# Kernel optimization log

Hardware: AMD Instinct MI355X
Metric: run time of the kernel (lower is better)

Reference implementation:

```python
import jax, jax.numpy as jnp
import numpy as np

NUM_EMBEDDINGS = 1024
EMBEDDING_DIM = 256
COMMITMENT_COST = 0.25
DECAY = 0.99
EPSILON = 1e-05


def setup_inputs() -> dict:
    key = jax.random.key(0)
    k1, k2, k3 = jax.random.split(key, 3)
    inputs = jax.random.normal(k1, (64, 1024, EMBEDDING_DIM), dtype=jnp.float32)
    embed_w = jax.random.uniform(
        k2, (NUM_EMBEDDINGS, EMBEDDING_DIM), dtype=jnp.float32,
        minval=-1.0 / NUM_EMBEDDINGS, maxval=1.0 / NUM_EMBEDDINGS)
    ema_cluster_size = jnp.ones((NUM_EMBEDDINGS,), dtype=jnp.float32)
    ema_w = jax.random.normal(k3, (NUM_EMBEDDINGS, EMBEDDING_DIM), dtype=jnp.float32)
    return {"inputs": inputs, "embed_w": embed_w,
            "ema_cluster_size": ema_cluster_size, "ema_w": ema_w}


def reference(inputs, embed_w, ema_cluster_size, ema_w):
    K, D = embed_w.shape
    flat = inputs.reshape(-1, D)  # [N, D]
    distances = (jnp.sum(flat * flat, axis=1, keepdims=True)
                 - 2.0 * flat @ embed_w.T
                 + jnp.sum(embed_w * embed_w, axis=1)[None, :])
    encoding_indices = jnp.argmin(distances, axis=1)  # [N]
    quantized = embed_w[encoding_indices].reshape(inputs.shape)

    # training-mode EMA updates (match torch buffer math; indices are constants)
    counts = jax.ops.segment_sum(
        jnp.ones_like(encoding_indices, dtype=inputs.dtype),
        encoding_indices, num_segments=K)  # == encodings.sum(0)
    dw = jax.ops.segment_sum(flat, encoding_indices, num_segments=K)  # == encodings.T @ flat
    new_cs = ema_cluster_size * DECAY + (1.0 - DECAY) * counts
    new_ema_w = ema_w * DECAY + (1.0 - DECAY) * dw
    n = jnp.sum(new_cs)
    new_cs = (new_cs + EPSILON) / (n + K * EPSILON) * n
    updated_embed = new_ema_w / new_cs[:, None]

    sg = jax.lax.stop_gradient
    e_latent_loss = jnp.mean((sg(quantized) - inputs) ** 2)
    q_latent_loss = jnp.mean((quantized - sg(inputs)) ** 2)
    loss = q_latent_loss + COMMITMENT_COST * e_latent_loss
    quantized_ste = inputs + sg(quantized - inputs)
    return (quantized_ste, loss, encoding_indices, new_cs, new_ema_w, updated_embed)
```

## Files before the change

### kernel.cpp

```cpp
#include <hip/hip_runtime.h>
#include <math.h>

#define NROWS 65536
#define D 256
#define K 1024
#define CAP 8
#define SCAP 16
#define EPS 1e-3f

#define OFF_Q     0
#define OFF_LOSS  16777216
#define OFF_IDX   16777217
#define OFF_CS    16842753
#define OFF_EMAW  16843777
#define OFF_UPD   17105921

#define WS_HIST     0
#define WS_GC       4096
#define WS_OFFS     8192
#define WS_CURS     12288
#define WS_IDX      16384
#define WS_CNT      278528
#define WS_WROWS    540672
#define WS_ROWIDS   802816
#define WS_SQX      1064960
#define WS_SQE      1327104
#define WS_DW       1331200
#define WS_PACK     1331200
#define WS_LOSSP    2379776
#define WS_EBT      2387968
#define WS_CAND     2912256

typedef __attribute__((ext_vector_type(8))) short short8;
typedef __attribute__((ext_vector_type(8))) unsigned short ushort8;
typedef __attribute__((ext_vector_type(4))) float f32x4;

__device__ __forceinline__ unsigned short f2b(float f) {
    unsigned u = __builtin_bit_cast(unsigned, f);
    return (unsigned short)((u + 0x7fffu + ((u >> 16) & 1u)) >> 16);
}

__device__ __forceinline__ float dot_chain(const float4* __restrict__ xr,
                                           const float4* __restrict__ er) {
#pragma clang fp contract(off)
    float acc = 0.f;
#pragma unroll
    for (int g = 0; g < 8; ++g) {
        float4 xa[8], ea[8];
#pragma unroll
        for (int m = 0; m < 8; ++m) { xa[m] = xr[g * 8 + m]; ea[m] = er[g * 8 + m]; }
#pragma unroll
        for (int m = 0; m < 8; ++m) {
            acc = __builtin_fmaf(xa[m].x, ea[m].x, acc);
            acc = __builtin_fmaf(xa[m].y, ea[m].y, acc);
            acc = __builtin_fmaf(xa[m].z, ea[m].z, acc);
            acc = __builtin_fmaf(xa[m].w, ea[m].w, acc);
        }
    }
    return acc;
}

__global__ __launch_bounds__(256) void k_cvt(const float* __restrict__ ew,
                                             unsigned short* __restrict__ ebt,
                                             float* __restrict__ sqe)
{
#pragma clang fp contract(off)
    int t = blockIdx.x * 256 + threadIdx.x;
    int code = t >> 3, kc = t & 7;
    const float4* src = (const float4*)&ew[(size_t)code * 256 + kc * 32];
    unsigned short* dst = &ebt[((size_t)kc * 1024 + code) * 32];
    float4 f[8];
#pragma unroll
    for (int j = 0; j < 8; ++j) f[j] = src[j];
#pragma unroll
    for (int j = 0; j < 8; ++j) {
        ushort4 o;
        o.x = f2b(f[j].x); o.y = f2b(f[j].y); o.z = f2b(f[j].z); o.w = f2b(f[j].w);
        *(ushort4*)&dst[j * 4] = o;
    }
    float p[16];
#pragma unroll
    for (int m = 0; m < 4; ++m) {
        p[4*m+0] = f[m].x * f[m].x + f[m+4].x * f[m+4].x;
        p[4*m+1] = f[m].y * f[m].y + f[m+4].y * f[m+4].y;
        p[4*m+2] = f[m].z * f[m].z + f[m+4].z * f[m+4].z;
        p[4*m+3] = f[m].w * f[m].w + f[m+4].w * f[m+4].w;
    }
    float V[16];
#pragma unroll
    for (int l2 = 0; l2 < 16; ++l2) {
        float q = p[l2] + __shfl_xor(p[l2], 1);
        V[l2] = q + __shfl_xor(q, 2);
    }
    float t8[8];
#pragma unroll
    for (int l2 = 0; l2 < 8; ++l2) t8[l2] = V[l2] + V[l2 + 8];
    float u4[4];
#pragma unroll
    for (int l2 = 0; l2 < 4; ++l2) u4[l2] = t8[l2] + t8[l2 + 4];
    float h = (u4[0] + u4[2]) + (u4[1] + u4[3]);
    float sq = h + __shfl_xor(h, 4);
    if (kc == 0) sqe[code] = sq;
}

__global__ __launch_bounds__(256) void k_screen(
    const float* __restrict__ x, const unsigned short* __restrict__ ebt,
    const float* __restrict__ sqe, float* __restrict__ sqx_out,
    int* __restrict__ cnt, int* __restrict__ cand,
    int* __restrict__ idx_out, float* __restrict__ idxf_out,
    int* __restrict__ hist, int* __restrict__ wrows, int* __restrict__ gc,
    unsigned long long* __restrict__ packed)
{
    __shared__ unsigned short xs[32][264];
    __shared__ float red[32][4];
    __shared__ int lcnt[32];
    __shared__ float gmin[32];
    __shared__ int scand_c[32][SCAP];
    __shared__ float scand_s[32][SCAP];

    const int tid = threadIdx.x;
    const int wn = tid >> 6;
    const int l = tid & 63;
    const int row0 = blockIdx.x * 32;

    if (tid < 32) { lcnt[tid] = 0; gmin[tid] = 3.4e38f; }

    {
        const int row = tid >> 3, kq8 = tid & 7;
        const float4* src = (const float4*)&x[(size_t)(row0 + row) * 256 + kq8 * 32];
        float4 f[8];
#pragma unroll
        for (int j = 0; j < 8; ++j) f[j] = src[j];
#pragma unroll
        for (int j = 0; j < 8; ++j) {
            ushort4 o;
            o.x = f2b(f[j].x); o.y = f2b(f[j].y); o.z = f2b(f[j].z); o.w = f2b(f[j].w);
            *(ushort4*)&xs[row][kq8 * 32 + j * 4] = o;
        }
        float p[16];
#pragma unroll
        for (int m = 0; m < 4; ++m) {
            p[4*m+0] = f[m].x * f[m].x + f[m+4].x * f[m+4].x;
            p[4*m+1] = f[m].y * f[m].y + f[m+4].y * f[m+4].y;
            p[4*m+2] = f[m].z * f[m].z + f[m+4].z * f[m+4].z;
            p[4*m+3] = f[m].w * f[m].w + f[m+4].w * f[m+4].w;
        }
        float V[16];
#pragma unroll
        for (int l2 = 0; l2 < 16; ++l2) {
            float q = p[l2] + __shfl_xor(p[l2], 1);
            V[l2] = q + __shfl_xor(q, 2);
        }
        float t8[8];
#pragma unroll
        for (int l2 = 0; l2 < 8; ++l2) t8[l2] = V[l2] + V[l2 + 8];
        float u4[4];
#pragma unroll
        for (int l2 = 0; l2 < 4; ++l2) u4[l2] = t8[l2] + t8[l2 + 4];
        float h = (u4[0] + u4[2]) + (u4[1] + u4[3]);
        float sq = h + __shfl_xor(h, 4);
        if (kq8 == 0) sqx_out[row0 + row] = sq;
    }
    __syncthreads();

#pragma unroll 1
    for (int ct = 0; ct < 4; ++ct) {
        f32x4 acc[2][4];
#pragma unroll
        for (int mt = 0; mt < 2; ++mt)
#pragma unroll
            for (int nt = 0; nt < 4; ++nt) acc[mt][nt] = (f32x4)0.f;

#pragma unroll 2
        for (int kc = 0; kc < 8; ++kc) {
            short8 a[2], b[4];
#pragma unroll
            for (int nt = 0; nt < 4; ++nt)
                b[nt] = *(const short8*)&ebt[
                    ((size_t)kc * 1024 + ct * 256 + wn * 64 + nt * 16 + (l & 15)) * 32
                    + (l >> 4) * 8];
#pragma unroll
            for (int mt = 0; mt < 2; ++mt)
                a[mt] = *(const short8*)&xs[mt * 16 + (l & 15)][kc * 32 + (l >> 4) * 8];
#pragma unroll
            for (int mt = 0; mt < 2; ++mt)
#pragma unroll
                for (int nt = 0; nt < 4; ++nt)
                    acc[mt][nt] = __builtin_amdgcn_mfma_f32_16x16x32_bf16(
                        a[mt], b[nt], acc[mt][nt], 0, 0, 0);
        }

        float sev[4];
#pragma unroll
        for (int nt = 0; nt < 4; ++nt)
            sev[nt] = sqe[ct * 256 + wn * 64 + nt * 16 + (l & 15)];

#pragma unroll
        for (int mt = 0; mt < 2; ++mt)
#pragma unroll
            for (int q = 0; q < 4; ++q) {
                const int rw = mt * 16 + (l >> 4) * 4 + q;
                float v = 3.4e38f;
#pragma unroll
                for (int nt = 0; nt < 4; ++nt)
                    v = fminf(v, sev[nt] - 2.0f * acc[mt][nt][q]);
#pragma unroll
                for (int m = 1; m < 16; m <<= 1) v = fminf(v, __shfl_xor(v, m));
                if ((l & 15) == 0) red[rw][wn] = v;
            }
        __syncthreads();
        if (tid < 32)
            gmin[tid] = fminf(gmin[tid],
                              fminf(fminf(red[tid][0], red[tid][1]),
                                    fminf(red[tid][2], red[tid][3])));
#pragma unroll
        for (int mt = 0; mt < 2; ++mt)
#pragma unroll
            for (int q = 0; q < 4; ++q) {
                const int rw = mt * 16 + (l >> 4) * 4 + q;
                const float rm = fminf(fminf(red[rw][0], red[rw][1]),
                                       fminf(red[rw][2], red[rw][3])) + EPS;
#pragma unroll
                for (int nt = 0; nt < 4; ++nt) {
                    float s = sev[nt] - 2.0f * acc[mt][nt][q];
                    if (s <= rm) {
                        int c = ct * 256 + wn * 64 + nt * 16 + (l & 15);
                        int slot = atomicAdd(&lcnt[rw], 1);
                        if (slot < SCAP) { scand_c[rw][slot] = c; scand_s[rw][slot] = s; }
                    }
                }
            }
        __syncthreads();
    }
    if (tid < 32) {
        const int row = row0 + tid;
        const int m = lcnt[tid];
        if (m > SCAP) {
            cnt[row] = CAP + 1;
            packed[row] = ~0ULL;
            int p0 = atomicAdd(&gc[0], 1);
            wrows[p0] = row;
        } else {
            const float thr = gmin[tid] + EPS;
            int n = 0;
            int keep[CAP];
            for (int j = 0; j < m; ++j) {
                if (scand_s[tid][j] <= thr) {
                    if (n < CAP) keep[n] = scand_c[tid][j];
                    ++n;
                }
            }
            cnt[row] = n;
            if (n == 1) {
                idx_out[row] = keep[0];
                idxf_out[row] = (float)keep[0];
                atomicAdd(&hist[keep[0]], 1);
            } else {
                packed[row] = ~0ULL;
                int p0 = atomicAdd(&gc[0], 1);
                wrows[p0] = row;
                const int mm = n < CAP ? n : CAP;
                for (int s = 0; s < mm; ++s)
                    cand[(size_t)row * CAP + s] = keep[s];
            }
        }
    }
}

__global__ __launch_bounds__(256) void k_rescore(
    const float* __restrict__ x, const float* __restrict__ ew,
    const float* __restrict__ sqx, const float* __restrict__ sqe,
    const int* __restrict__ cnt, const int* __restrict__ cand,
    const int* __restrict__ wrows, const int* __restrict__ gc,
    unsigned long long* __restrict__ packed)
{
#pragma clang fp contract(off)
    const int nw = gc[0];
    const int total = nw * CAP;
    for (int i = blockIdx.x * 256 + threadIdx.x; i < total; i += gridDim.x * 256) {
        const int row = wrows[i >> 3];
        const int slot = i & (CAP - 1);
        const int n = cnt[row];
        const float sxr = sqx[row];
        const float4* xr = (const float4*)&x[(size_t)row * 256];
        if (n >= 2 && n <= CAP) {
            if (slot >= n) continue;
            const int c = cand[(size_t)row * CAP + slot];
            float acc = dot_chain(xr, (const float4*)&ew[(size_t)c * 256]);
            float d = (sxr - 2.0f * acc) + sqe[c];
            unsigned long long key =
                ((unsigned long long)__builtin_bit_cast(unsigned, d) << 32) | (unsigned)c;
            atomicMin(&packed[row], key);
        } else {
            float bd = 3.4e38f; int bc = 0x7fffffff;
            for (int c = slot; c < K; c += CAP) {
                float acc = dot_chain(xr, (const float4*)&ew[(size_t)c * 256]);
                float d = (sxr - 2.0f * acc) + sqe[c];
                if (d < bd || (d == bd && c < bc)) { bd = d; bc = c; }
            }
            unsigned long long key =
                ((unsigned long long)__builtin_bit_cast(unsigned, bd) << 32) | (unsigned)bc;
            atomicMin(&packed[row], key);
        }
    }
}

__global__ __launch_bounds__(256) void k_resolve(
    const int* __restrict__ wrows, const int* __restrict__ gc,
    const unsigned long long* __restrict__ packed,
    int* __restrict__ idx_out, float* __restrict__ idxf_out, int* __restrict__ hist)
{
    const int nw = gc[0];
    for (int i = blockIdx.x * 256 + threadIdx.x; i < nw; i += gridDim.x * 256) {
        const int row = wrows[i];
        const int c = (int)(packed[row] & 0xffffffffu);
        idx_out[row] = c;
        idxf_out[row] = (float)c;
        atomicAdd(&hist[c], 1);
    }
}

__global__ __launch_bounds__(1024) void k_prefix(
    const int* __restrict__ hist, int* __restrict__ offs, int* __restrict__ curs)
{
    __shared__ int tmp[1024];
    const int tid = threadIdx.x;
    const int h = hist[tid];
    tmp[tid] = h;
    __syncthreads();
    for (int off = 1; off < 1024; off <<= 1) {
        int v = (tid >= off) ? tmp[tid - off] : 0;
        __syncthreads();
        tmp[tid] += v;
        __syncthreads();
    }
    int ex = tmp[tid] - h;
    offs[tid] = ex;
    curs[tid] = ex;
}

__global__ __launch_bounds__(256) void k_fill(
    const int* __restrict__ idx_in, int* __restrict__ curs, int* __restrict__ rowids)
{
    int r = blockIdx.x * 256 + threadIdx.x;
    int c = idx_in[r];
    int slot = atomicAdd(&curs[c], 1);
    rowids[slot] = r;
}

__global__ __launch_bounds__(256) void k_dw(
    const float* __restrict__ x, const float* __restrict__ ew,
    const int* __restrict__ hist, const int* __restrict__ offs,
    const int* __restrict__ rowids,
    float* __restrict__ q_out, float* __restrict__ dw, double* __restrict__ lossp)
{
    const int c = blockIdx.x;
    const int tid = threadIdx.x;
    const int n = hist[c];
    const int base = offs[c];
    const float ev = ew[(size_t)c * 256 + tid];
    float acc = 0.f;
    float lsum = 0.f;
    for (int i = 0; i < n; ++i) {
        int row = rowids[base + i];
        float xv = x[(size_t)row * 256 + tid];
        q_out[(size_t)row * 256 + tid] = ev;
        acc += xv;
        float df = ev - xv;
        lsum += df * df;
    }
    dw[(size_t)c * 256 + tid] = acc;
    const int lane = tid & 63, wid = tid >> 6;
    __shared__ float wsum[4];
#pragma unroll
    for (int m = 1; m < 64; m <<= 1) lsum += __shfl_xor(lsum, m);
    if (lane == 0) wsum[wid] = lsum;
    __syncthreads();
    if (tid == 0)
        lossp[c] = (double)wsum[0] + wsum[1] + wsum[2] + wsum[3];
}

__global__ __launch_bounds__(1024) void k_finalize(
    const float* __restrict__ ema_cs, const int* __restrict__ hist,
    const double* __restrict__ lossp, float* __restrict__ out)
{
    __shared__ double red[1024];
    const int tid = threadIdx.x;
    float raw = ema_cs[tid] * 0.99f + 0.01f * (float)hist[tid];
    red[tid] = (double)raw;
    __syncthreads();
    for (int s = 512; s > 0; s >>= 1) {
        if (tid < s) red[tid] += red[tid + s];
        __syncthreads();
    }
    double n = red[0];
    __syncthreads();
    float csn = (raw + 1e-5f) * (float)(n / (n + 1024.0 * 1e-5));
    out[OFF_CS + tid] = csn;
    red[tid] = lossp[tid];
    __syncthreads();
    for (int s = 512; s > 0; s >>= 1) {
        if (tid < s) red[tid] += red[tid + s];
        __syncthreads();
    }
    if (tid == 0) out[OFF_LOSS] = (float)(red[0] * 1.25 / 16777216.0);
}

__global__ __launch_bounds__(256) void k_ema(
    const float* __restrict__ ema_w, const float* __restrict__ dw,
    const float* __restrict__ cs_out, float* __restrict__ out)
{
    int id = blockIdx.x * 256 + threadIdx.x;
    int k = id >> 8;
    float nw = ema_w[id] * 0.99f + 0.01f * dw[id];
    out[OFF_EMAW + id] = nw;
    out[OFF_UPD + id] = nw / cs_out[k];
}

extern "C" void kernel_launch(void* const* d_in, const int* in_sizes, int n_in,
                              void* d_out, int out_size, void* d_ws, size_t ws_size,
                              hipStream_t stream)
{
    const float* x      = (const float*)d_in[0];
    const float* ew     = (const float*)d_in[1];
    const float* ema_cs = (const float*)d_in[2];
    const float* ema_w  = (const float*)d_in[3];
    float* out = (float*)d_out;
    char* ws = (char*)d_ws;

    int*    hist    = (int*)(ws + WS_HIST);
    int*    gc      = (int*)(ws + WS_GC);
    int*    offs    = (int*)(ws + WS_OFFS);
    int*    curs    = (int*)(ws + WS_CURS);
    int*    idxi    = (int*)(ws + WS_IDX);
    int*    cnt     = (int*)(ws + WS_CNT);
    int*    wrows   = (int*)(ws + WS_WROWS);
    int*    rowids  = (int*)(ws + WS_ROWIDS);
    float*  sqx     = (float*)(ws + WS_SQX);
    float*  sqe     = (float*)(ws + WS_SQE);
    float*  dw      = (float*)(ws + WS_DW);
    unsigned long long* packed = (unsigned long long*)(ws + WS_PACK);
    double* lossp   = (double*)(ws + WS_LOSSP);
    unsigned short* ebt = (unsigned short*)(ws + WS_EBT);
    int*    cand    = (int*)(ws + WS_CAND);

    hipMemsetAsync(ws, 0, 4112, stream);
    hipLaunchKernelGGL(k_cvt, dim3(32), dim3(256), 0, stream, ew, ebt, sqe);
    hipLaunchKernelGGL(k_screen, dim3(NROWS / 32), dim3(256), 0, stream,
                       x, ebt, sqe, sqx, cnt, cand, idxi, out + OFF_IDX,
                       hist, wrows, gc, packed);
    hipLaunchKernelGGL(k_rescore, dim3(512), dim3(256), 0, stream,
                       x, ew, sqx, sqe, cnt, cand, wrows, gc, packed);
    hipLaunchKernelGGL(k_resolve, dim3(64), dim3(256), 0, stream,
                       wrows, gc, packed, idxi, out + OFF_IDX, hist);
    hipLaunchKernelGGL(k_prefix, dim3(1), dim3(1024), 0, stream, hist, offs, curs);
    hipLaunchKernelGGL(k_fill, dim3(NROWS / 256), dim3(256), 0, stream,
                       idxi, curs, rowids);
    hipLaunchKernelGGL(k_dw, dim3(K), dim3(256), 0, stream,
                       x, ew, hist, offs, rowids, out + OFF_Q, dw, lossp);
    hipLaunchKernelGGL(k_finalize, dim3(1), dim3(1024), 0, stream,
                       ema_cs, hist, lossp, out);
    hipLaunchKernelGGL(k_ema, dim3(1024), dim3(256), 0, stream,
                       ema_w, dw, out + OFF_CS, out);
}
```

Before: 196.2 us.

## Split per-code dw gather into 64-row work units to balance load

The gather/segment-sum kernel previously ran one block per code, so a code with many assigned rows serialized its whole gather in a single block. Codes are now split into chunks of up to 64 rows, and the chunk list is built in the prefix kernel. Each chunk writes a partial dw row and a loss partial, and the EMA kernel sums the partials per code. This adds a second scan, extra workspace traffic and a fixed grid of 2048 blocks, which is only correct if the chunk count never exceeds 2048.

```diff
diff --git a/kernel.cpp b/kernel.cpp
--- a/kernel.cpp
+++ b/kernel.cpp
@@ -19,17 +19,19 @@
 #define WS_GC       4096
 #define WS_OFFS     8192
 #define WS_CURS     12288
-#define WS_IDX      16384
-#define WS_CNT      278528
-#define WS_WROWS    540672
-#define WS_ROWIDS   802816
-#define WS_SQX      1064960
-#define WS_SQE      1327104
-#define WS_DW       1331200
-#define WS_PACK     1331200
-#define WS_LOSSP    2379776
-#define WS_EBT      2387968
-#define WS_CAND     2912256
+#define WS_UOFFS    16384
+#define WS_UNITS    20736
+#define WS_IDX      29184
+#define WS_CNT      291328
+#define WS_WROWS    553472
+#define WS_ROWIDS   815616
+#define WS_SQX      1077760
+#define WS_SQE      1339904
+#define WS_LOSSP    1344000
+#define WS_EBT      1360384
+#define WS_CAND     1884672
+#define WS_UDW      3981824
+#define WS_PACK     3981824
 
 typedef __attribute__((ext_vector_type(8))) short short8;
 typedef __attribute__((ext_vector_type(8))) unsigned short ushort8;
@@ -321,7 +323,8 @@
 }
 
 __global__ __launch_bounds__(1024) void k_prefix(
-    const int* __restrict__ hist, int* __restrict__ offs, int* __restrict__ curs)
+    const int* __restrict__ hist, int* __restrict__ offs, int* __restrict__ curs,
+    int* __restrict__ uoffs, int* __restrict__ units, double* __restrict__ lossp)
 {
     __shared__ int tmp[1024];
     const int tid = threadIdx.x;
@@ -337,6 +340,23 @@
     int ex = tmp[tid] - h;
     offs[tid] = ex;
     curs[tid] = ex;
+    __syncthreads();
+    const int uc = (h + 63) >> 6;
+    tmp[tid] = uc;
+    __syncthreads();
+    for (int off = 1; off < 1024; off <<= 1) {
+        int v = (tid >= off) ? tmp[tid - off] : 0;
+        __syncthreads();
+        tmp[tid] += v;
+        __syncthreads();
+    }
+    const int uex = tmp[tid] - uc;
+    uoffs[tid] = uex;
+    if (tid == 1023) uoffs[1024] = tmp[1023];
+    lossp[tid] = 0.0;
+    lossp[tid + 1024] = 0.0;
+    for (int j = 0; j < uc; ++j)
+        units[uex + j] = (j << 10) | tid;
 }
 
 __global__ __launch_bounds__(256) void k_fill(
@@ -351,17 +371,25 @@
 __global__ __launch_bounds__(256) void k_dw(
     const float* __restrict__ x, const float* __restrict__ ew,
     const int* __restrict__ hist, const int* __restrict__ offs,
+    const int* __restrict__ uoffs, const int* __restrict__ units,
     const int* __restrict__ rowids,
-    float* __restrict__ q_out, float* __restrict__ dw, double* __restrict__ lossp)
-{
-    const int c = blockIdx.x;
+    float* __restrict__ q_out, float* __restrict__ udw, double* __restrict__ lossp)
+{
+    const int U = uoffs[1024];
+    const int b = blockIdx.x;
+    if (b >= U) return;
+    const int u = units[b];
+    const int c = u & 1023;
+    const int j = u >> 10;
     const int tid = threadIdx.x;
     const int n = hist[c];
-    const int base = offs[c];
+    const int start = j << 6;
+    const int len = min(64, n - start);
+    const int base = offs[c] + start;
     const float ev = ew[(size_t)c * 256 + tid];
     float acc = 0.f;
     float lsum = 0.f;
-    for (int i = 0; i < n; ++i) {
+    for (int i = 0; i < len; ++i) {
         int row = rowids[base + i];
         float xv = x[(size_t)row * 256 + tid];
         q_out[(size_t)row * 256 + tid] = ev;
@@ -369,7 +397,7 @@
         float df = ev - xv;
         lsum += df * df;
     }
-    dw[(size_t)c * 256 + tid] = acc;
+    udw[(size_t)b * 256 + tid] = acc;
     const int lane = tid & 63, wid = tid >> 6;
     __shared__ float wsum[4];
 #pragma unroll
@@ -377,7 +405,7 @@
     if (lane == 0) wsum[wid] = lsum;
     __syncthreads();
     if (tid == 0)
-        lossp[c] = (double)wsum[0] + wsum[1] + wsum[2] + wsum[3];
+        lossp[b] = (double)wsum[0] + wsum[1] + wsum[2] + wsum[3];
 }
 
 __global__ __launch_bounds__(1024) void k_finalize(
@@ -397,7 +425,7 @@
     __syncthreads();
     float csn = (raw + 1e-5f) * (float)(n / (n + 1024.0 * 1e-5));
     out[OFF_CS + tid] = csn;
-    red[tid] = lossp[tid];
+    red[tid] = lossp[tid] + lossp[tid + 1024];
     __syncthreads();
     for (int s = 512; s > 0; s >>= 1) {
         if (tid < s) red[tid] += red[tid + s];
@@ -407,14 +435,19 @@
 }
 
 __global__ __launch_bounds__(256) void k_ema(
-    const float* __restrict__ ema_w, const float* __restrict__ dw,
+    const float* __restrict__ ema_w, const float* __restrict__ udw,
+    const int* __restrict__ uoffs,
     const float* __restrict__ cs_out, float* __restrict__ out)
 {
     int id = blockIdx.x * 256 + threadIdx.x;
-    int k = id >> 8;
-    float nw = ema_w[id] * 0.99f + 0.01f * dw[id];
+    int c = id >> 8;
+    int d = id & 255;
+    const int u0 = uoffs[c], u1 = uoffs[c + 1];
+    float s = 0.f;
+    for (int u = u0; u < u1; ++u) s += udw[(size_t)u * 256 + d];
+    float nw = ema_w[id] * 0.99f + 0.01f * s;
     out[OFF_EMAW + id] = nw;
-    out[OFF_UPD + id] = nw / cs_out[k];
+    out[OFF_UPD + id] = nw / cs_out[c];
 }
 
 extern "C" void kernel_launch(void* const* d_in, const int* in_sizes, int n_in,
@@ -432,13 +465,15 @@
     int*    gc      = (int*)(ws + WS_GC);
     int*    offs    = (int*)(ws + WS_OFFS);
     int*    curs    = (int*)(ws + WS_CURS);
+    int*    uoffs   = (int*)(ws + WS_UOFFS);
+    int*    units   = (int*)(ws + WS_UNITS);
     int*    idxi    = (int*)(ws + WS_IDX);
     int*    cnt     = (int*)(ws + WS_CNT);
     int*    wrows   = (int*)(ws + WS_WROWS);
     int*    rowids  = (int*)(ws + WS_ROWIDS);
     float*  sqx     = (float*)(ws + WS_SQX);
     float*  sqe     = (float*)(ws + WS_SQE);
-    float*  dw      = (float*)(ws + WS_DW);
+    float*  udw     = (float*)(ws + WS_UDW);
     unsigned long long* packed = (unsigned long long*)(ws + WS_PACK);
     double* lossp   = (double*)(ws + WS_LOSSP);
     unsigned short* ebt = (unsigned short*)(ws + WS_EBT);
@@ -453,13 +488,15 @@
                        x, ew, sqx, sqe, cnt, cand, wrows, gc, packed);
     hipLaunchKernelGGL(k_resolve, dim3(64), dim3(256), 0, stream,
                        wrows, gc, packed, idxi, out + OFF_IDX, hist);
-    hipLaunchKernelGGL(k_prefix, dim3(1), dim3(1024), 0, stream, hist, offs, curs);
+    hipLaunchKernelGGL(k_prefix, dim3(1), dim3(1024), 0, stream,
+                       hist, offs, curs, uoffs, units, lossp);
     hipLaunchKernelGGL(k_fill, dim3(NROWS / 256), dim3(256), 0, stream,
                        idxi, curs, rowids);
-    hipLaunchKernelGGL(k_dw, dim3(K), dim3(256), 0, stream,
-                       x, ew, hist, offs, rowids, out + OFF_Q, dw, lossp);
+    hipLaunchKernelGGL(k_dw, dim3(2048), dim3(256), 0, stream,
+                       x, ew, hist, offs, uoffs, units, rowids,
+                       out + OFF_Q, udw, lossp);
     hipLaunchKernelGGL(k_finalize, dim3(1), dim3(1024), 0, stream,
                        ema_cs, hist, lossp, out);
     hipLaunchKernelGGL(k_ema, dim3(1024), dim3(256), 0, stream,
-                       ema_w, dw, out + OFF_CS, out);
-}
+                       ema_w, udw, uoffs, out + OFF_CS, out);
+}
```

Result: faster. 176.3 us (-10.1%).
